# Performance work log

Hardware: AMD Instinct MI355X
Metric: run time of the kernel (lower is better)

## Reference

```python
import jax, jax.numpy as jnp
import numpy as np

B, C, H, W = 16, 512, 32, 32
KC = C // 8  # key_channels = 64


def setup_inputs() -> dict:
    key = jax.random.key(0)
    ks = jax.random.split(key, 6)
    s_in = 1.0 / np.sqrt(C)
    return {
        "x": jax.random.normal(ks[0], (B, C, H, W), dtype=jnp.float32),
        "Wq": jax.random.normal(ks[1], (KC, C), dtype=jnp.float32) * s_in,
        "bq": jnp.zeros((KC,), dtype=jnp.float32),
        "Wk": jax.random.normal(ks[2], (KC, C), dtype=jnp.float32) * s_in,
        "bk": jnp.zeros((KC,), dtype=jnp.float32),
        "Wv": jax.random.normal(ks[3], (C, C), dtype=jnp.float32) * s_in,
        "bv": jnp.zeros((C,), dtype=jnp.float32),
        "Wo": jax.random.normal(ks[4], (C, C), dtype=jnp.float32) * s_in,
        "bo": jnp.zeros((C,), dtype=jnp.float32),
        "gamma": jnp.zeros((1,), dtype=jnp.float32),
    }


def reference(x, Wq, bq, Wk, bk, Wv, bv, Wo, bo, gamma):
    b, c, h, w = x.shape
    n = h * w
    kc = Wq.shape[0]
    xf = x.reshape(b, c, n)  # [B, C, N]
    # 1x1 convs == channel matmuls
    q = jnp.einsum('kc,bcn->bnk', Wq, xf) + bq  # [B, N, KC]
    k = jnp.einsum('kc,bcn->bkn', Wk, xf) + bk[None, :, None]  # [B, KC, N]
    v = jnp.einsum('vc,bcn->bnv', Wv, xf) + bv  # [B, N, C]
    scale = jnp.asarray(kc, x.dtype) ** -0.5
    att = jax.nn.softmax(jnp.einsum('bnk,bkm->bnm', q, k) * scale, axis=-1)  # [B, N, N]
    out = jnp.einsum('bnm,bmv->bnv', att, v)  # [B, N, C]
    out = jnp.einsum('cv,bnv->bcn', Wo, out) + bo[None, :, None]  # [B, C, N]
    out = gamma[0] * out + xf
    return out.reshape(b, c, h, w)
```

## Files before the change

kernel.cpp:

```cpp
#include <hip/hip_runtime.h>
#include <cstddef>


typedef unsigned short ushort_t;
typedef __attribute__((ext_vector_type(8))) short bf16x8;
typedef __attribute__((ext_vector_type(4))) float f32x4;

__device__ __forceinline__ ushort_t f2bf(float f) {
  unsigned int x = __float_as_uint(f);
  unsigned int r = (x + 0x7fffu + ((x >> 16) & 1u)) >> 16;
  return (ushort_t)r;
}

__device__ __forceinline__ void gload16(const ushort_t* g, ushort_t* l) {
  __builtin_amdgcn_global_load_lds(
      (const __attribute__((address_space(1))) void*)g,
      (__attribute__((address_space(3))) void*)l, 16, 0, 0);
}

template <int TM>
__device__ __forceinline__ void gemm_core(
    const ushort_t* __restrict__ A, int lda,
    const ushort_t* __restrict__ B, int ldb,
    int K, int m0, int n0,
    ushort_t* As, ushort_t* Bs, f32x4 (*acc)[4])
{
  constexpr int MT  = TM / 32;
  constexpr int WTM = TM / 2;
  const int t = threadIdx.x;
  const int lane = t & 63, quad = lane >> 4, l15 = lane & 15;
  const int w = t >> 6, wm = w >> 1, wn = w & 1;
  const int rr = (lane >> 3) & 7;
  const int gg = (lane & 7) ^ rr;

  #pragma unroll
  for (int i = 0; i < MT; ++i)
    #pragma unroll
    for (int j = 0; j < 4; ++j) acc[i][j] = (f32x4){0.f, 0.f, 0.f, 0.f};

  for (int k0 = 0; k0 < K; k0 += 64) {
    #pragma unroll
    for (int i = 0; i < TM / 32; ++i) {
      const int mrow = w * (TM / 4) + i * 8;
      gload16(A + (size_t)(m0 + mrow + rr) * lda + k0 + gg * 8,
              As + mrow * 64);
    }
    #pragma unroll
    for (int i = 0; i < 4; ++i) {
      const int mrow = w * 32 + i * 8;
      gload16(B + (size_t)(n0 + mrow + rr) * ldb + k0 + gg * 8,
              Bs + mrow * 64);
    }
    __syncthreads();
    #pragma unroll
    for (int kk = 0; kk < 2; ++kk) {
      const int gq = kk * 4 + quad;
      const int sg = (gq ^ (l15 & 7)) * 8;
      bf16x8 af[MT], bfr[4];
      #pragma unroll
      for (int i = 0; i < MT; ++i)
        af[i] = *(const bf16x8*)(As + (wm * WTM + i * 16 + l15) * 64 + sg);
      #pragma unroll
      for (int j = 0; j < 4; ++j)
        bfr[j] = *(const bf16x8*)(Bs + (wn * 64 + j * 16 + l15) * 64 + sg);
      #pragma unroll
      for (int i = 0; i < MT; ++i)
        #pragma unroll
        for (int j = 0; j < 4; ++j)
          acc[i][j] = __builtin_amdgcn_mfma_f32_16x16x32_bf16(
              af[i], bfr[j], acc[i][j], 0, 0, 0);
    }
    __syncthreads();
  }
}

template <int TM, class F>
__device__ __forceinline__ void store_bf16(
    ushort_t* lds, ushort_t* __restrict__ out, int ldo, int m0, int n0,
    f32x4 (*acc)[4], F f)
{
  constexpr int MT = TM / 32, WTM = TM / 2, SI = TM / 16;
  const int t = threadIdx.x;
  const int lane = t & 63, quad = lane >> 4, l15 = lane & 15;
  const int w = t >> 6, wm = w >> 1, wn = w & 1;
  #pragma unroll
  for (int i = 0; i < MT; ++i)
    #pragma unroll
    for (int j = 0; j < 4; ++j)
      #pragma unroll
      for (int r = 0; r < 4; ++r) {
        const int rl = wm * WTM + i * 16 + quad * 4 + r;
        const int cl = wn * 64 + j * 16 + l15;
        lds[rl * 136 + cl] = f2bf(f(i, j, r, rl, cl, acc[i][j][r]));
      }
  __syncthreads();
  #pragma unroll
  for (int i = 0; i < SI; ++i) {
    const int s = i * 256 + t, m = s >> 4, g = s & 15;
    const uint4 v = *(const uint4*)(lds + m * 136 + g * 8);
    *(uint4*)(out + (size_t)(m0 + m) * ldo + n0 + g * 8) = v;
  }
}

__global__ __launch_bounds__(256) void prep_x(
    const float* __restrict__ x, ushort_t* __restrict__ xbfT)
{
  __shared__ float T[64][65];
  const int t = threadIdx.x;
  const int b = blockIdx.z, c0 = blockIdx.y * 64, n0 = blockIdx.x * 64;
  const float* xb = x + ((size_t)b * 512 + c0) * 1024 + n0;
  const int nj = t & 63, ci0 = t >> 6;
  #pragma unroll
  for (int p = 0; p < 16; ++p) {
    const int ci = p * 4 + ci0;
    T[ci][nj] = xb[(size_t)ci * 1024 + nj];
  }
  __syncthreads();
  const int c2 = (t & 31) * 2, nr0 = t >> 5;
  #pragma unroll
  for (int p = 0; p < 8; ++p) {
    const int nr = p * 8 + nr0;
    const unsigned lo = f2bf(T[c2][nr]), hi = f2bf(T[c2 + 1][nr]);
    *(unsigned*)&xbfT[((size_t)b * 1024 + n0 + nr) * 512 + c0 + c2] =
        lo | (hi << 16);
  }
}

__global__ __launch_bounds__(256) void wcvt(
    const float* __restrict__ Wq, const float* __restrict__ Wk,
    const float* __restrict__ Wv, const float* __restrict__ Wo,
    ushort_t* __restrict__ Wqk, ushort_t* __restrict__ Wvb,
    ushort_t* __restrict__ Wob)
{
  const int i = blockIdx.x * 256 + threadIdx.x;
  if (i < 65536) {
    const float v = (i < 32768) ? Wq[i] : Wk[i - 32768];
    Wqk[i] = f2bf(v);
  } else if (i < 327680) {
    Wvb[i - 65536] = f2bf(Wv[i - 65536]);
  } else if (i < 589824) {
    Wob[i - 327680] = f2bf(Wo[i - 327680]);
  }
}

__global__ __launch_bounds__(256) void k1a_qk(
    const ushort_t* __restrict__ xbfT, const ushort_t* __restrict__ Wqk,
    const float* __restrict__ bq, const float* __restrict__ bk,
    ushort_t* __restrict__ qkt)
{
  __shared__ __align__(16) ushort_t lds[(64 + 128) * 64];
  const int b = blockIdx.z, m0 = blockIdx.y * 64;
  f32x4 acc[2][4];
  gemm_core<64>(xbfT + (size_t)b * 524288, 512, Wqk, 512, 512, m0, 0,
                lds, lds + 64 * 64, acc);
  const int t = threadIdx.x, lane = t & 63, l15 = lane & 15;
  const int w = t >> 6, wn = w & 1;
  float bc[4];
  #pragma unroll
  for (int j = 0; j < 4; ++j) {
    const int col = wn * 64 + j * 16 + l15;
    bc[j] = (col < 64) ? bq[col] : bk[col - 64];
  }
  store_bf16<64>(lds, qkt + (size_t)b * 131072, 128, m0, 0, acc,
      [&](int, int j, int, int, int, float v) { return v + bc[j]; });
}

__global__ __launch_bounds__(256) void k1b_v(
    const ushort_t* __restrict__ Wvb, const ushort_t* __restrict__ xbfT,
    const float* __restrict__ bv, ushort_t* __restrict__ vt2)
{
  __shared__ __align__(16) ushort_t lds[128 * 136];
  const int b = blockIdx.z, m0 = blockIdx.y * 128, n0 = blockIdx.x * 128;
  f32x4 acc[4][4];
  gemm_core<128>(Wvb, 512, xbfT + (size_t)b * 524288, 512, 512, m0, n0,
                 lds, lds + 128 * 64, acc);
  const int t = threadIdx.x, lane = t & 63, quad = lane >> 4;
  const int w = t >> 6, wm = w >> 1;
  float br[4][4];
  #pragma unroll
  for (int i = 0; i < 4; ++i)
    #pragma unroll
    for (int r = 0; r < 4; ++r)
      br[i][r] = bv[m0 + wm * 64 + i * 16 + quad * 4 + r];
  store_bf16<128>(lds, vt2 + (size_t)b * 524288, 1024, m0, n0, acc,
      [&](int i, int, int r, int, int, float v) { return v + br[i][r]; });
}

__global__ __launch_bounds__(256) void k2_scores(
    const ushort_t* __restrict__ qkt, ushort_t* __restrict__ p,
    float* __restrict__ lpart)
{
  __shared__ __align__(16) ushort_t lds[128 * 136];
  __shared__ float lsum[128][2];
  const int b = blockIdx.z, m0 = blockIdx.y * 128, c0 = blockIdx.x * 128;
  f32x4 acc[4][4];
  const ushort_t* A = qkt + (size_t)b * 131072;
  gemm_core<128>(A, 128, A + 64, 128, 64, m0, c0, lds, lds + 128 * 64, acc);
  const int t = threadIdx.x, lane = t & 63, quad = lane >> 4, l15 = lane & 15;
  const int w = t >> 6, wm = w >> 1, wn = w & 1;
  #pragma unroll
  for (int i = 0; i < 4; ++i)
    #pragma unroll
    for (int r = 0; r < 4; ++r) {
      float s = 0.f;
      #pragma unroll
      for (int j = 0; j < 4; ++j) {
        const float e = __expf(acc[i][j][r] * 0.125f);
        acc[i][j][r] = e;
        s += e;
      }
      #pragma unroll
      for (int d = 1; d < 16; d <<= 1) s += __shfl_xor(s, d);
      if (l15 == 0) lsum[wm * 64 + i * 16 + quad * 4 + r][wn] = s;
    }
  store_bf16<128>(lds, p + (size_t)b * 1048576, 1024, m0, c0, acc,
      [](int, int, int, int, int, float v) { return v; });
  if (t < 128)
    lpart[(size_t)b * 8192 + (size_t)blockIdx.x * 1024 + m0 + t] =
        lsum[t][0] + lsum[t][1];
}

__global__ void k2b_rowsum(const float* __restrict__ lpart,
                           float* __restrict__ linv)
{
  const int b = blockIdx.x, n = threadIdx.x;
  float s = 0.f;
  #pragma unroll
  for (int ct = 0; ct < 8; ++ct) s += lpart[(size_t)b * 8192 + ct * 1024 + n];
  linv[b * 1024 + n] = 1.0f / s;
}

__global__ __launch_bounds__(256) void k3_pv(
    const ushort_t* __restrict__ p, const ushort_t* __restrict__ vt2,
    const float* __restrict__ linv, ushort_t* __restrict__ o1)
{
  __shared__ __align__(16) ushort_t lds[128 * 136];
  const int b = blockIdx.z, m0 = blockIdx.y * 128, c0 = blockIdx.x * 128;
  f32x4 acc[4][4];
  gemm_core<128>(p + (size_t)b * 1048576, 1024, vt2 + (size_t)b * 524288, 1024,
                 1024, m0, c0, lds, lds + 128 * 64, acc);
  const int t = threadIdx.x, lane = t & 63, quad = lane >> 4;
  const int w = t >> 6, wm = w >> 1;
  float li[4][4];
  #pragma unroll
  for (int i = 0; i < 4; ++i)
    #pragma unroll
    for (int r = 0; r < 4; ++r)
      li[i][r] = linv[b * 1024 + m0 + wm * 64 + i * 16 + quad * 4 + r];
  store_bf16<128>(lds, o1 + (size_t)b * 524288, 512, m0, c0, acc,
      [&](int i, int, int r, int, int, float v) { return v * li[i][r]; });
}

__global__ __launch_bounds__(256) void k4_proj(
    const ushort_t* __restrict__ Wob, const ushort_t* __restrict__ o1,
    const float* __restrict__ bo, const float* __restrict__ gamma,
    const float* __restrict__ x, float* __restrict__ out)
{
  __shared__ __align__(16) ushort_t lds[128 * 136];
  const int b = blockIdx.z, m0 = blockIdx.y * 128, n0 = blockIdx.x * 128;
  f32x4 acc[4][4];
  gemm_core<128>(Wob, 512, o1 + (size_t)b * 524288, 512, 512, m0, n0,
                 lds, lds + 128 * 64, acc);
  const int t = threadIdx.x, lane = t & 63, quad = lane >> 4, l15 = lane & 15;
  const int w = t >> 6, wm = w >> 1, wn = w & 1;
  const float g = gamma[0];
  float br[4][4];
  #pragma unroll
  for (int i = 0; i < 4; ++i)
    #pragma unroll
    for (int r = 0; r < 4; ++r)
      br[i][r] = bo[m0 + wm * 64 + i * 16 + quad * 4 + r];
  float* fl = (float*)lds;
  #pragma unroll
  for (int h = 0; h < 2; ++h) {
    if (wm == h) {
      #pragma unroll
      for (int i = 0; i < 4; ++i)
        #pragma unroll
        for (int j = 0; j < 4; ++j)
          #pragma unroll
          for (int r = 0; r < 4; ++r)
            fl[(i * 16 + quad * 4 + r) * 132 + wn * 64 + j * 16 + l15] =
                g * (acc[i][j][r] + br[i][r]);
    }
    __syncthreads();
    #pragma unroll
    for (int i2 = 0; i2 < 8; ++i2) {
      const int s = i2 * 256 + t, m = s >> 5, c4 = s & 31;
      f32x4 v = *(const f32x4*)(fl + m * 132 + c4 * 4);
      const size_t gi = ((size_t)b * 512 + m0 + h * 64 + m) * 1024 + n0 + c4 * 4;
      const f32x4 xr = *(const f32x4*)(x + gi);
      v += xr;
      *(f32x4*)(out + gi) = v;
    }
    __syncthreads();
  }
}

extern "C" void kernel_launch(void* const* d_in, const int* in_sizes, int n_in,
                              void* d_out, int out_size, void* d_ws, size_t ws_size,
                              hipStream_t stream) {
  const float* x     = (const float*)d_in[0];
  const float* Wq    = (const float*)d_in[1];
  const float* bq    = (const float*)d_in[2];
  const float* Wk    = (const float*)d_in[3];
  const float* bk    = (const float*)d_in[4];
  const float* Wv    = (const float*)d_in[5];
  const float* bv    = (const float*)d_in[6];
  const float* Wo    = (const float*)d_in[7];
  const float* bo    = (const float*)d_in[8];
  const float* gamma = (const float*)d_in[9];
  float* out = (float*)d_out;

  char* wsp = (char*)d_ws;
  ushort_t* xbfT   = (ushort_t*)wsp;  wsp += (size_t)16 * 1024 * 512 * 2;
  ushort_t* Wqk_bf = (ushort_t*)wsp;  wsp += (size_t)128 * 512 * 2;
  ushort_t* Wv_bf  = (ushort_t*)wsp;  wsp += (size_t)512 * 512 * 2;
  ushort_t* Wo_bf  = (ushort_t*)wsp;  wsp += (size_t)512 * 512 * 2;
  ushort_t* qkt    = (ushort_t*)wsp;  wsp += (size_t)16 * 1024 * 128 * 2;
  ushort_t* vt2    = (ushort_t*)wsp;  wsp += (size_t)16 * 512 * 1024 * 2;
  ushort_t* p      = (ushort_t*)wsp;  wsp += (size_t)16 * 1024 * 1024 * 2;
  float*    lpart  = (float*)wsp;     wsp += (size_t)16 * 8 * 1024 * 4;
  float*    linv   = (float*)wsp;     wsp += (size_t)16 * 1024 * 4;
  ushort_t* o1     = xbfT;

  prep_x    <<<dim3(16, 8, 16), 256, 0, stream>>>(x, xbfT);
  wcvt      <<<2304, 256, 0, stream>>>(Wq, Wk, Wv, Wo, Wqk_bf, Wv_bf, Wo_bf);
  k1a_qk    <<<dim3(1, 16, 16), 256, 0, stream>>>(xbfT, Wqk_bf, bq, bk, qkt);
  k1b_v     <<<dim3(8, 4, 16), 256, 0, stream>>>(Wv_bf, xbfT, bv, vt2);
  k2_scores <<<dim3(8, 8, 16), 256, 0, stream>>>(qkt, p, lpart);
  k2b_rowsum<<<16, 1024, 0, stream>>>(lpart, linv);
  k3_pv     <<<dim3(4, 8, 16), 256, 0, stream>>>(p, vt2, linv, o1);
  k4_proj   <<<dim3(8, 4, 16), 256, 0, stream>>>(Wo_bf, o1, bo, gamma, x, out);
}
```

Before: 197.4 us.

## Fuse scores, softmax and PV into flash-style attention kernel; merge prep launches

Replaces the separate score, row-sum and PV kernels with one flash-style kernel. Each block computes exp(QK^T) for a 64-key chunk into LDS, accumulates row sums and multiplies by V, so the 32 MB bf16 P matrix is never written to or read from global memory. It also folds weight conversion into prep_x as extra blocks and merges the QK and V projection GEMMs into one launch, cutting the launch count from 8 to 4. The trade-off is that the attention kernel recomputes scores for each of its 2 channel halves and runs with smaller tiles and more barriers per chunk. Like the previous code it skips the max subtraction in the softmax.

```diff
diff --git a/kernel.cpp b/kernel.cpp
--- a/kernel.cpp
+++ b/kernel.cpp
@@ -42,14 +42,12 @@
     #pragma unroll
     for (int i = 0; i < TM / 32; ++i) {
       const int mrow = w * (TM / 4) + i * 8;
-      gload16(A + (size_t)(m0 + mrow + rr) * lda + k0 + gg * 8,
-              As + mrow * 64);
+      gload16(A + (size_t)(m0 + mrow + rr) * lda + k0 + gg * 8, As + mrow * 64);
     }
     #pragma unroll
     for (int i = 0; i < 4; ++i) {
       const int mrow = w * 32 + i * 8;
-      gload16(B + (size_t)(n0 + mrow + rr) * ldb + k0 + gg * 8,
-              Bs + mrow * 64);
+      gload16(B + (size_t)(n0 + mrow + rr) * ldb + k0 + gg * 8, Bs + mrow * 64);
     }
     __syncthreads();
     #pragma unroll
@@ -103,10 +101,35 @@
 }
 
 __global__ __launch_bounds__(256) void prep_x(
-    const float* __restrict__ x, ushort_t* __restrict__ xbfT)
+    const float* __restrict__ x,
+    const float* __restrict__ Wq, const float* __restrict__ Wk,
+    const float* __restrict__ Wv, const float* __restrict__ Wo,
+    ushort_t* __restrict__ xbfT, ushort_t* __restrict__ Wqk,
+    ushort_t* __restrict__ Wvb, ushort_t* __restrict__ Wob)
 {
   __shared__ float T[64][65];
   const int t = threadIdx.x;
+  if (blockIdx.y == 8) {
+    const int id = blockIdx.z * 16 + blockIdx.x;
+    #pragma unroll
+    for (int p = 0; p < 5; ++p) {
+      const int s = p * 256 + t;
+      if (s < 1152) {
+        const int u = id * 1152 + s;
+        const int e = u * 2;
+        float f0, f1;
+        if (e < 32768)       { f0 = Wq[e];         f1 = Wq[e + 1]; }
+        else if (e < 65536)  { f0 = Wk[e - 32768]; f1 = Wk[e - 32767]; }
+        else if (e < 327680) { f0 = Wv[e - 65536]; f1 = Wv[e - 65535]; }
+        else                 { f0 = Wo[e - 327680]; f1 = Wo[e - 327679]; }
+        const unsigned pk = (unsigned)f2bf(f0) | ((unsigned)f2bf(f1) << 16);
+        if (e < 65536)       *((unsigned*)Wqk + u) = pk;
+        else if (e < 327680) *((unsigned*)Wvb + (u - 32768)) = pk;
+        else                 *((unsigned*)Wob + (u - 163840)) = pk;
+      }
+    }
+    return;
+  }
   const int b = blockIdx.z, c0 = blockIdx.y * 64, n0 = blockIdx.x * 64;
   const float* xb = x + ((size_t)b * 512 + c0) * 1024 + n0;
   const int nj = t & 63, ci0 = t >> 6;
@@ -126,129 +149,181 @@
   }
 }
 
-__global__ __launch_bounds__(256) void wcvt(
-    const float* __restrict__ Wq, const float* __restrict__ Wk,
-    const float* __restrict__ Wv, const float* __restrict__ Wo,
-    ushort_t* __restrict__ Wqk, ushort_t* __restrict__ Wvb,
-    ushort_t* __restrict__ Wob)
-{
-  const int i = blockIdx.x * 256 + threadIdx.x;
-  if (i < 65536) {
-    const float v = (i < 32768) ? Wq[i] : Wk[i - 32768];
-    Wqk[i] = f2bf(v);
-  } else if (i < 327680) {
-    Wvb[i - 65536] = f2bf(Wv[i - 65536]);
-  } else if (i < 589824) {
-    Wob[i - 327680] = f2bf(Wo[i - 327680]);
-  }
-}
-
-__global__ __launch_bounds__(256) void k1a_qk(
+__global__ __launch_bounds__(256) void k1_fused(
     const ushort_t* __restrict__ xbfT, const ushort_t* __restrict__ Wqk,
+    const ushort_t* __restrict__ Wvb,
     const float* __restrict__ bq, const float* __restrict__ bk,
-    ushort_t* __restrict__ qkt)
-{
-  __shared__ __align__(16) ushort_t lds[(64 + 128) * 64];
-  const int b = blockIdx.z, m0 = blockIdx.y * 64;
-  f32x4 acc[2][4];
-  gemm_core<64>(xbfT + (size_t)b * 524288, 512, Wqk, 512, 512, m0, 0,
-                lds, lds + 64 * 64, acc);
-  const int t = threadIdx.x, lane = t & 63, l15 = lane & 15;
-  const int w = t >> 6, wn = w & 1;
-  float bc[4];
-  #pragma unroll
-  for (int j = 0; j < 4; ++j) {
-    const int col = wn * 64 + j * 16 + l15;
-    bc[j] = (col < 64) ? bq[col] : bk[col - 64];
-  }
-  store_bf16<64>(lds, qkt + (size_t)b * 131072, 128, m0, 0, acc,
-      [&](int, int j, int, int, int, float v) { return v + bc[j]; });
-}
-
-__global__ __launch_bounds__(256) void k1b_v(
-    const ushort_t* __restrict__ Wvb, const ushort_t* __restrict__ xbfT,
-    const float* __restrict__ bv, ushort_t* __restrict__ vt2)
-{
-  __shared__ __align__(16) ushort_t lds[128 * 136];
-  const int b = blockIdx.z, m0 = blockIdx.y * 128, n0 = blockIdx.x * 128;
-  f32x4 acc[4][4];
-  gemm_core<128>(Wvb, 512, xbfT + (size_t)b * 524288, 512, 512, m0, n0,
-                 lds, lds + 128 * 64, acc);
-  const int t = threadIdx.x, lane = t & 63, quad = lane >> 4;
-  const int w = t >> 6, wm = w >> 1;
-  float br[4][4];
-  #pragma unroll
-  for (int i = 0; i < 4; ++i)
-    #pragma unroll
-    for (int r = 0; r < 4; ++r)
-      br[i][r] = bv[m0 + wm * 64 + i * 16 + quad * 4 + r];
-  store_bf16<128>(lds, vt2 + (size_t)b * 524288, 1024, m0, n0, acc,
-      [&](int i, int, int r, int, int, float v) { return v + br[i][r]; });
-}
-
-__global__ __launch_bounds__(256) void k2_scores(
-    const ushort_t* __restrict__ qkt, ushort_t* __restrict__ p,
-    float* __restrict__ lpart)
-{
-  __shared__ __align__(16) ushort_t lds[128 * 136];
-  __shared__ float lsum[128][2];
-  const int b = blockIdx.z, m0 = blockIdx.y * 128, c0 = blockIdx.x * 128;
-  f32x4 acc[4][4];
-  const ushort_t* A = qkt + (size_t)b * 131072;
-  gemm_core<128>(A, 128, A + 64, 128, 64, m0, c0, lds, lds + 128 * 64, acc);
+    const float* __restrict__ bv,
+    ushort_t* __restrict__ qkt, ushort_t* __restrict__ vt2)
+{
+  __shared__ __align__(16) ushort_t lds[17408];
+  const int bid = blockIdx.x;
   const int t = threadIdx.x, lane = t & 63, quad = lane >> 4, l15 = lane & 15;
   const int w = t >> 6, wm = w >> 1, wn = w & 1;
-  #pragma unroll
-  for (int i = 0; i < 4; ++i)
+  if (bid < 512) {
+    const int b = bid >> 5, my = (bid >> 3) & 3, nx = bid & 7;
+    const int m0 = my * 128, n0 = nx * 128;
+    f32x4 acc[4][4];
+    gemm_core<128>(Wvb, 512, xbfT + (size_t)b * 524288, 512, 512, m0, n0,
+                   lds, lds + 128 * 64, acc);
+    float br[4][4];
+    #pragma unroll
+    for (int i = 0; i < 4; ++i)
+      #pragma unroll
+      for (int r = 0; r < 4; ++r)
+        br[i][r] = bv[m0 + wm * 64 + i * 16 + quad * 4 + r];
+    store_bf16<128>(lds, vt2 + (size_t)b * 524288, 1024, m0, n0, acc,
+        [&](int i, int, int r, int, int, float v) { return v + br[i][r]; });
+  } else {
+    const int id = bid - 512, b = id >> 4, my = id & 15;
+    const int m0 = my * 64;
+    f32x4 acc[2][4];
+    gemm_core<64>(xbfT + (size_t)b * 524288, 512, Wqk, 512, 512, m0, 0,
+                  lds, lds + 64 * 64, acc);
+    float bc[4];
+    #pragma unroll
+    for (int j = 0; j < 4; ++j) {
+      const int col = wn * 64 + j * 16 + l15;
+      bc[j] = (col < 64) ? bq[col] : bk[col - 64];
+    }
+    store_bf16<64>(lds, qkt + (size_t)b * 131072, 128, m0, 0, acc,
+        [&](int, int j, int, int, int, float v) { return v + bc[j]; });
+  }
+}
+
+__global__ __launch_bounds__(256) void flash_attn(
+    const ushort_t* __restrict__ qkt, const ushort_t* __restrict__ vt2,
+    ushort_t* __restrict__ o1)
+{
+  __shared__ __align__(16) ushort_t buf[29184];
+  __shared__ float lsum[64][2];
+  ushort_t* Qs = buf;
+  ushort_t* Ks = buf + 4096;
+  ushort_t* Vs = buf + 8192;
+  ushort_t* Ps = buf + 24576;
+
+  const int t = threadIdx.x;
+  const int lane = t & 63, quad = lane >> 4, l15 = lane & 15;
+  const int w = t >> 6, wm = w >> 1, wn = w & 1;
+  const int rr = (lane >> 3) & 7, gg = (lane & 7) ^ rr;
+
+  const int b = blockIdx.z, m0 = blockIdx.y * 64, c0 = blockIdx.x * 256;
+  const ushort_t* qb = qkt + (size_t)b * 131072;
+  const ushort_t* vb = vt2 + (size_t)b * 524288;
+
+  #pragma unroll
+  for (int i = 0; i < 2; ++i) {
+    const int mrow = w * 16 + i * 8;
+    gload16(qb + (size_t)(m0 + mrow + rr) * 128 + gg * 8, Qs + mrow * 64);
+  }
+
+  f32x4 accO[2][8];
+  #pragma unroll
+  for (int i = 0; i < 2; ++i)
+    #pragma unroll
+    for (int j = 0; j < 8; ++j) accO[i][j] = (f32x4){0.f, 0.f, 0.f, 0.f};
+  float rsum[2][4] = {{0.f, 0.f, 0.f, 0.f}, {0.f, 0.f, 0.f, 0.f}};
+
+  #pragma unroll 1
+  for (int mc = 0; mc < 1024; mc += 64) {
+    __syncthreads();
+    #pragma unroll
+    for (int i = 0; i < 2; ++i) {
+      const int mrow = w * 16 + i * 8;
+      gload16(qb + (size_t)(mc + mrow + rr) * 128 + 64 + gg * 8, Ks + mrow * 64);
+    }
+    #pragma unroll
+    for (int i = 0; i < 8; ++i) {
+      const int mrow = w * 64 + i * 8;
+      gload16(vb + (size_t)(c0 + mrow + rr) * 1024 + mc + gg * 8, Vs + mrow * 64);
+    }
+    __syncthreads();
+
+    f32x4 accS[2][2];
+    #pragma unroll
+    for (int i = 0; i < 2; ++i)
+      #pragma unroll
+      for (int j = 0; j < 2; ++j) accS[i][j] = (f32x4){0.f, 0.f, 0.f, 0.f};
+    #pragma unroll
+    for (int kk = 0; kk < 2; ++kk) {
+      const int gq = kk * 4 + quad;
+      const int sg = (gq ^ (l15 & 7)) * 8;
+      bf16x8 af[2], bfr[2];
+      #pragma unroll
+      for (int i = 0; i < 2; ++i)
+        af[i] = *(const bf16x8*)(Qs + (wm * 32 + i * 16 + l15) * 64 + sg);
+      #pragma unroll
+      for (int j = 0; j < 2; ++j)
+        bfr[j] = *(const bf16x8*)(Ks + (wn * 32 + j * 16 + l15) * 64 + sg);
+      #pragma unroll
+      for (int i = 0; i < 2; ++i)
+        #pragma unroll
+        for (int j = 0; j < 2; ++j)
+          accS[i][j] = __builtin_amdgcn_mfma_f32_16x16x32_bf16(
+              af[i], bfr[j], accS[i][j], 0, 0, 0);
+    }
+    #pragma unroll
+    for (int i = 0; i < 2; ++i)
+      #pragma unroll
+      for (int j = 0; j < 2; ++j)
+        #pragma unroll
+        for (int r = 0; r < 4; ++r) {
+          const float e = __expf(accS[i][j][r] * 0.125f);
+          rsum[i][r] += e;
+          Ps[(wm * 32 + i * 16 + quad * 4 + r) * 72 + wn * 32 + j * 16 + l15] =
+              f2bf(e);
+        }
+    __syncthreads();
+
+    #pragma unroll
+    for (int kk = 0; kk < 2; ++kk) {
+      const int gq = kk * 4 + quad;
+      const int sgv = (gq ^ (l15 & 7)) * 8;
+      bf16x8 af[2], bfr[8];
+      #pragma unroll
+      for (int i = 0; i < 2; ++i)
+        af[i] = *(const bf16x8*)(Ps + (wm * 32 + i * 16 + l15) * 72 + gq * 8);
+      #pragma unroll
+      for (int j = 0; j < 8; ++j)
+        bfr[j] = *(const bf16x8*)(Vs + (wn * 128 + j * 16 + l15) * 64 + sgv);
+      #pragma unroll
+      for (int i = 0; i < 2; ++i)
+        #pragma unroll
+        for (int j = 0; j < 8; ++j)
+          accO[i][j] = __builtin_amdgcn_mfma_f32_16x16x32_bf16(
+              af[i], bfr[j], accO[i][j], 0, 0, 0);
+    }
+  }
+
+  #pragma unroll
+  for (int i = 0; i < 2; ++i)
     #pragma unroll
     for (int r = 0; r < 4; ++r) {
-      float s = 0.f;
-      #pragma unroll
-      for (int j = 0; j < 4; ++j) {
-        const float e = __expf(acc[i][j][r] * 0.125f);
-        acc[i][j][r] = e;
-        s += e;
-      }
-      #pragma unroll
-      for (int d = 1; d < 16; d <<= 1) s += __shfl_xor(s, d);
-      if (l15 == 0) lsum[wm * 64 + i * 16 + quad * 4 + r][wn] = s;
-    }
-  store_bf16<128>(lds, p + (size_t)b * 1048576, 1024, m0, c0, acc,
-      [](int, int, int, int, int, float v) { return v; });
-  if (t < 128)
-    lpart[(size_t)b * 8192 + (size_t)blockIdx.x * 1024 + m0 + t] =
-        lsum[t][0] + lsum[t][1];
-}
-
-__global__ void k2b_rowsum(const float* __restrict__ lpart,
-                           float* __restrict__ linv)
-{
-  const int b = blockIdx.x, n = threadIdx.x;
-  float s = 0.f;
-  #pragma unroll
-  for (int ct = 0; ct < 8; ++ct) s += lpart[(size_t)b * 8192 + ct * 1024 + n];
-  linv[b * 1024 + n] = 1.0f / s;
-}
-
-__global__ __launch_bounds__(256) void k3_pv(
-    const ushort_t* __restrict__ p, const ushort_t* __restrict__ vt2,
-    const float* __restrict__ linv, ushort_t* __restrict__ o1)
-{
-  __shared__ __align__(16) ushort_t lds[128 * 136];
-  const int b = blockIdx.z, m0 = blockIdx.y * 128, c0 = blockIdx.x * 128;
-  f32x4 acc[4][4];
-  gemm_core<128>(p + (size_t)b * 1048576, 1024, vt2 + (size_t)b * 524288, 1024,
-                 1024, m0, c0, lds, lds + 128 * 64, acc);
-  const int t = threadIdx.x, lane = t & 63, quad = lane >> 4;
-  const int w = t >> 6, wm = w >> 1;
-  float li[4][4];
-  #pragma unroll
-  for (int i = 0; i < 4; ++i)
-    #pragma unroll
-    for (int r = 0; r < 4; ++r)
-      li[i][r] = linv[b * 1024 + m0 + wm * 64 + i * 16 + quad * 4 + r];
-  store_bf16<128>(lds, o1 + (size_t)b * 524288, 512, m0, c0, acc,
-      [&](int i, int, int r, int, int, float v) { return v * li[i][r]; });
+      float s = rsum[i][r];
+      #pragma unroll
+      for (int d = 1; d < 16; d <<= 1) s += __shfl_xor(s, d, 16);
+      if (l15 == 0) lsum[wm * 32 + i * 16 + quad * 4 + r][wn] = s;
+    }
+  __syncthreads();
+
+  ushort_t* fl_b = buf + 4096;
+  #pragma unroll
+  for (int i = 0; i < 2; ++i)
+    #pragma unroll
+    for (int r = 0; r < 4; ++r) {
+      const int row = wm * 32 + i * 16 + quad * 4 + r;
+      const float inv = 1.0f / (lsum[row][0] + lsum[row][1]);
+      #pragma unroll
+      for (int j = 0; j < 8; ++j)
+        fl_b[row * 264 + wn * 128 + j * 16 + l15] = f2bf(accO[i][j][r] * inv);
+    }
+  __syncthreads();
+  #pragma unroll
+  for (int p = 0; p < 8; ++p) {
+    const int s = p * 256 + t, m = s >> 5, g = s & 31;
+    const uint4 v = *(const uint4*)(fl_b + m * 264 + g * 8);
+    *(uint4*)(o1 + ((size_t)b * 1024 + m0 + m) * 512 + c0 + g * 8) = v;
+  }
 }
 
 __global__ __launch_bounds__(256) void k4_proj(
@@ -319,17 +394,11 @@
   ushort_t* Wo_bf  = (ushort_t*)wsp;  wsp += (size_t)512 * 512 * 2;
   ushort_t* qkt    = (ushort_t*)wsp;  wsp += (size_t)16 * 1024 * 128 * 2;
   ushort_t* vt2    = (ushort_t*)wsp;  wsp += (size_t)16 * 512 * 1024 * 2;
-  ushort_t* p      = (ushort_t*)wsp;  wsp += (size_t)16 * 1024 * 1024 * 2;
-  float*    lpart  = (float*)wsp;     wsp += (size_t)16 * 8 * 1024 * 4;
-  float*    linv   = (float*)wsp;     wsp += (size_t)16 * 1024 * 4;
   ushort_t* o1     = xbfT;
 
-  prep_x    <<<dim3(16, 8, 16), 256, 0, stream>>>(x, xbfT);
-  wcvt      <<<2304, 256, 0, stream>>>(Wq, Wk, Wv, Wo, Wqk_bf, Wv_bf, Wo_bf);
-  k1a_qk    <<<dim3(1, 16, 16), 256, 0, stream>>>(xbfT, Wqk_bf, bq, bk, qkt);
-  k1b_v     <<<dim3(8, 4, 16), 256, 0, stream>>>(Wv_bf, xbfT, bv, vt2);
-  k2_scores <<<dim3(8, 8, 16), 256, 0, stream>>>(qkt, p, lpart);
-  k2b_rowsum<<<16, 1024, 0, stream>>>(lpart, linv);
-  k3_pv     <<<dim3(4, 8, 16), 256, 0, stream>>>(p, vt2, linv, o1);
+  prep_x    <<<dim3(16, 9, 16), 256, 0, stream>>>(x, Wq, Wk, Wv, Wo,
+                                                  xbfT, Wqk_bf, Wv_bf, Wo_bf);
+  k1_fused  <<<768, 256, 0, stream>>>(xbfT, Wqk_bf, Wv_bf, bq, bk, bv, qkt, vt2);
+  flash_attn<<<dim3(2, 16, 16), 256, 0, stream>>>(qkt, vt2, o1);
   k4_proj   <<<dim3(8, 4, 16), 256, 0, stream>>>(Wo_bf, o1, bo, gamma, x, out);
 }
```

New measurement: 184.8 us. 1.07x faster.
